# Optimization experiments

Hardware: AMD Instinct MI355X
Metric: run time of the kernel (lower is better)

## Reference

```python
import jax, jax.numpy as jnp
import numpy as np
import math

D_MODEL = 512
EXPAND = 1
D_INNER = EXPAND * D_MODEL          # 512
HALF = D_INNER // 2                 # 256 per-branch channels
D_STATE = D_MODEL // 4 * EXPAND     # 128 (overrides d_state arg in __init__)
DT_RANK = math.ceil(D_MODEL / 16)   # 32
D_CONV = 4


def _dwconv_same(x, w):
    # x: (B, C, L), w: (C, 1, k); torch padding='same' for k=4 -> pad (left=1, right=2)
    k = w.shape[-1]
    total = k - 1
    left = total // 2
    return jax.lax.conv_general_dilated(
        x, w, window_strides=(1,), padding=[(left, total - left)],
        feature_group_count=w.shape[0], dimension_numbers=("NCH", "OIH", "NCH"))


def _sparse_approx(m):
    thr = jnp.max(m) * 0.1
    return jnp.sign(m) * jax.nn.relu(jnp.abs(m) - thr)


def _selective_scan(u, delta, A, Bc, Cc, D):
    # u, delta: (B, d, L); A: (d, n); Bc, Cc: (B, n, L); D: (d,)
    dT = jnp.moveaxis(delta, 2, 0)   # (L, B, d)
    uT = jnp.moveaxis(u, 2, 0)       # (L, B, d)
    BT = jnp.moveaxis(Bc, 2, 0)      # (L, B, n)
    CT = jnp.moveaxis(Cc, 2, 0)      # (L, B, n)

    def step(h, inputs):
        d_t, u_t, b_t, c_t = inputs                      # (B,d),(B,d),(B,n),(B,n)
        dA = jnp.exp(d_t[..., None] * A)                 # (B, d, n)
        dBu = d_t[..., None] * b_t[:, None, :] * u_t[..., None]
        h = dA * h + dBu                                 # (B, d, n)
        y = jnp.einsum("bdn,bn->bd", h, c_t)
        return h, y

    h0 = jnp.zeros((u.shape[0], u.shape[1], A.shape[1]), dtype=u.dtype)
    _, ys = jax.lax.scan(step, h0, (dT, uT, BT, CT))     # ys: (L, B, d)
    y = jnp.moveaxis(ys, 0, 2)                           # (B, d, L)
    return y + u * D[:, None]


def _branch(inph, in_w, cx_w, cz_w, xproj_w, dt_w, dt_b, out_w, A, D):
    # inph: (B, L, d_model)
    xz = jnp.swapaxes(inph @ in_w.T, 1, 2)   # (B, d_inner, L)
    x, z = xz[:, :HALF], xz[:, HALF:]
    x = jax.nn.silu(_dwconv_same(x, cx_w))   # (B, half, L); conv bias is False (True//2==0)
    z = jax.nn.silu(_dwconv_same(z, cz_w))
    x_dbl = jnp.swapaxes(x, 1, 2) @ xproj_w.T        # (B, L, dt_rank + 2n)
    dt = x_dbl[..., :DT_RANK] @ dt_w.T               # (B, L, half)
    dt = jnp.swapaxes(dt, 1, 2)                      # (B, half, L)
    Bc = jnp.swapaxes(x_dbl[..., DT_RANK:DT_RANK + D_STATE], 1, 2)   # (B, n, L)
    Cc = jnp.swapaxes(x_dbl[..., DT_RANK + D_STATE:], 1, 2)          # (B, n, L)
    Bc = _sparse_approx(Bc)
    Cc = _sparse_approx(Cc)
    delta = jax.nn.softplus(dt + dt_b[None, :, None])
    y = _selective_scan(x, delta, A, Bc, Cc, D)
    out = jnp.concatenate([y, z], axis=1)            # (B, d_inner, L)
    return jnp.swapaxes(out, 1, 2) @ out_w.T         # (B, L, d_model)


def setup_inputs() -> dict:
    key = jax.random.key(0)
    ks = jax.random.split(key, 16)
    B, L = 2, 2048
    s = lambda fan: 1.0 / np.sqrt(fan)

    inp = jax.random.normal(ks[0], (B, 2 * D_MODEL, L), jnp.float32)

    in_proj_w = jax.random.uniform(ks[1], (D_INNER, D_MODEL), jnp.float32, -s(D_MODEL), s(D_MODEL))
    x_proj_w = jax.random.uniform(ks[2], (DT_RANK + 2 * D_STATE, HALF), jnp.float32, -s(HALF), s(HALF))
    dt_init_std = DT_RANK ** (-0.5)
    dt_proj_w = jax.random.uniform(ks[3], (HALF, DT_RANK), jnp.float32, -dt_init_std, dt_init_std)
    out_proj_w = jax.random.uniform(ks[4], (D_MODEL, D_INNER), jnp.float32, -s(D_INNER), s(D_INNER))

    in_proj_2_w = jax.random.uniform(ks[5], (D_INNER, D_MODEL), jnp.float32, -s(D_MODEL), s(D_MODEL))
    x_proj_2_w = jax.random.uniform(ks[6], (DT_RANK + 2 * D_STATE, HALF), jnp.float32, -s(HALF), s(HALF))
    dt_proj_2_w = jax.random.uniform(ks[7], (HALF, DT_RANK), jnp.float32, -dt_init_std, dt_init_std)
    out_proj_2_w = jax.random.uniform(ks[8], (D_MODEL, D_INNER), jnp.float32, -s(D_INNER), s(D_INNER))

    # dt bias init: inverse-softplus of dt ~ LogUniform(1e-3, 1e-1), floor 1e-4
    def inv_softplus_dt(k):
        u = jax.random.uniform(k, (HALF,), jnp.float32)
        dt = jnp.exp(u * (np.log(0.1) - np.log(0.001)) + np.log(0.001))
        dt = jnp.clip(dt, 1e-4, None)
        return dt + jnp.log(-jnp.expm1(-dt))
    dt_proj_b = inv_softplus_dt(ks[9])
    dt_proj_2_b = inv_softplus_dt(ks[10])

    cs = 1.0 / np.sqrt(D_CONV)  # depthwise conv fan_in = 1*k
    conv_x_w = jax.random.uniform(ks[11], (HALF, 1, D_CONV), jnp.float32, -cs, cs)
    conv_z_w = jax.random.uniform(ks[12], (HALF, 1, D_CONV), jnp.float32, -cs, cs)
    conv_x_2_w = jax.random.uniform(ks[13], (HALF, 1, D_CONV), jnp.float32, -cs, cs)
    conv_z_2_w = jax.random.uniform(ks[14], (HALF, 1, D_CONV), jnp.float32, -cs, cs)

    A_log = jnp.log(jnp.broadcast_to(jnp.arange(1, D_STATE + 1, dtype=jnp.float32), (HALF, D_STATE)))
    D = jnp.ones((HALF,), jnp.float32)
    epsilon = jnp.array([0.01], jnp.float32)

    return dict(inp=inp, in_proj_w=in_proj_w, conv_x_w=conv_x_w, conv_z_w=conv_z_w,
                x_proj_w=x_proj_w, dt_proj_w=dt_proj_w, dt_proj_b=dt_proj_b, out_proj_w=out_proj_w,
                in_proj_2_w=in_proj_2_w, conv_x_2_w=conv_x_2_w, conv_z_2_w=conv_z_2_w,
                x_proj_2_w=x_proj_2_w, dt_proj_2_w=dt_proj_2_w, dt_proj_2_b=dt_proj_2_b,
                out_proj_2_w=out_proj_2_w, A_log=A_log, D=D, epsilon=epsilon)


def reference(inp, in_proj_w, conv_x_w, conv_z_w, x_proj_w, dt_proj_w, dt_proj_b, out_proj_w,
              in_proj_2_w, conv_x_2_w, conv_z_2_w, x_proj_2_w, dt_proj_2_w, dt_proj_2_b,
              out_proj_2_w, A_log, D, epsilon):
    # inp: (B, 2*d_model, L) -> split along dim 1, permute to (B, L, d_model)
    inpx = jnp.swapaxes(inp[:, :D_MODEL, :], 1, 2)
    inpy = jnp.swapaxes(inp[:, D_MODEL:, :], 1, 2)

    A_base = (1.0 + epsilon[0]) * (-jnp.exp(A_log))
    A1 = _sparse_approx(A_base)        # branch 1
    A2 = _sparse_approx(A1)            # branch 2 sparsifies the already-sparsified A

    out1 = _branch(inpx, in_proj_w, conv_x_w, conv_z_w, x_proj_w, dt_proj_w, dt_proj_b, out_proj_w, A1, D)
    out2 = _branch(inpy, in_proj_2_w, conv_x_2_w, conv_z_2_w, x_proj_2_w, dt_proj_2_w, dt_proj_2_b, out_proj_2_w, A2, D)
    return out1, out2
```

## Files before the change

kernel.cpp:

```cpp
#include <hip/hip_runtime.h>
#include <math.h>

constexpr int B_    = 2;
constexpr int L_    = 2048;
constexpr int NROW  = B_ * L_;
constexpr int MROW  = 2 * NROW;
constexpr int HALF_ = 256;
constexpr int DS_   = 128;

constexpr float LOG2E = 1.4426950408889634f;

constexpr size_t OFF_MINP = 0;
constexpr size_t OFF_BCMX = 32;
constexpr size_t OFF_XZ   = 64;
constexpr size_t OFF_YT   = OFF_XZ + (size_t)MROW * 256;
constexpr size_t OFF_XDBL = OFF_XZ + (size_t)MROW * 512;
constexpr size_t OFF_XS   = OFF_XDBL + (size_t)MROW * 288;
constexpr size_t OFF_BS   = OFF_XS  + (size_t)MROW * 256;
constexpr size_t OFF_CS   = OFF_BS  + (size_t)2 * NROW * 128;
constexpr size_t OFF_DTT  = OFF_CS  + (size_t)2 * NROW * 128;
constexpr size_t OFF_DUT  = OFF_DTT + (size_t)2 * 256 * 4096;
constexpr size_t OFF_UDT  = OFF_DUT + (size_t)2 * 256 * 4096;
constexpr size_t FLOAT_END = OFF_UDT + (size_t)2 * 256 * 4096;

constexpr size_t HOFF_XINH = 0;
constexpr size_t HOFF_XINL = HOFF_XINH + (size_t)MROW * 512;
constexpr size_t HOFF_YZH  = HOFF_XINH;
constexpr size_t HOFF_YZL  = HOFF_XINL;
constexpr size_t HOFF_XSH  = HOFF_XINL + (size_t)MROW * 512;
constexpr size_t HOFF_XSL  = HOFF_XSH  + (size_t)MROW * 256;
constexpr size_t HOFF_INWH = HOFF_XSL  + (size_t)MROW * 256;
constexpr size_t HOFF_INWL = HOFF_INWH + 524288;
constexpr size_t HOFF_XWH  = HOFF_INWL + 524288;
constexpr size_t HOFF_XWL  = HOFF_XWH  + 147456;
constexpr size_t HOFF_OUTWH= HOFF_XWL  + 147456;
constexpr size_t HOFF_OUTWL= HOFF_OUTWH+ 524288;

constexpr size_t WST_IN = 262144;
constexpr size_t WST_X  = 73728;

constexpr int PRE_MINA = 32;
constexpr int PRE_WSPL = (1196032 + 255) / 256;
constexpr int PRE_TIN  = 64 * 16 * 4;
constexpr int PRE_BLOCKS = PRE_MINA + PRE_WSPL + PRE_TIN;

typedef __bf16 bf16x8 __attribute__((ext_vector_type(8)));
typedef float  f32x4  __attribute__((ext_vector_type(4)));

__device__ __forceinline__ unsigned short bf16rn(float x) {
    unsigned u = __float_as_uint(x);
    unsigned r = (u + 0x7FFFu + ((u >> 16) & 1u)) >> 16;
    return (unsigned short)r;
}
__device__ __forceinline__ void split2(float x, unsigned short& h, unsigned short& l) {
    h = bf16rn(x);
    float hf = __uint_as_float(((unsigned)h) << 16);
    l = bf16rn(x - hf);
}

__device__ __forceinline__ float shrinkf(float v, float thr) {
    float a = fabsf(v) - thr;
    a = fmaxf(a, 0.0f);
    float r = copysignf(a, v);
    return (v == 0.0f) ? 0.0f : r;
}
__device__ __forceinline__ float siluf(float v) { return v / (1.0f + __expf(-v)); }
__device__ __forceinline__ float softplusf(float v) {
    return fmaxf(v, 0.0f) + log1pf(__expf(-fabsf(v)));
}
__device__ __forceinline__ float rlanef(float v, int l) {
    return __int_as_float(__builtin_amdgcn_readlane(__float_as_int(v), l));
}
__device__ __forceinline__ unsigned fkey(float f) {
    unsigned u = __float_as_uint(f);
    return (u >> 31) ? ~u : (u | 0x80000000u);
}
__device__ __forceinline__ float funkey(unsigned k) {
    unsigned u = (k >> 31) ? (k & 0x7FFFFFFFu) : ~k;
    return __uint_as_float(u);
}

__global__ __launch_bounds__(256) void pre_all(const float* __restrict__ A_log,
                                               const float* __restrict__ inp,
                                               const float* __restrict__ in_w0,
                                               const float* __restrict__ in_w1,
                                               const float* __restrict__ outw0,
                                               const float* __restrict__ outw1,
                                               const float* __restrict__ xw0,
                                               const float* __restrict__ xw1,
                                               float* __restrict__ ws,
                                               unsigned* __restrict__ bcmax,
                                               unsigned short* __restrict__ hb) {
    int bid = blockIdx.x;
    int tid = threadIdx.x;
    if (bid < PRE_MINA) {
        __shared__ float sbuf[8];
        int i = bid * 1024 + tid * 4;
        float4 v = *(const float4*)(A_log + i);
        float mv = fminf(fminf(v.x, v.y), fminf(v.z, v.w));
        #pragma unroll
        for (int off = 32; off > 0; off >>= 1) mv = fminf(mv, __shfl_xor(mv, off));
        if ((tid & 63) == 0) sbuf[tid >> 6] = mv;
        __syncthreads();
        if (tid == 0) {
            float r = fminf(fminf(sbuf[0], sbuf[1]), fminf(sbuf[2], sbuf[3]));
            ws[OFF_MINP + bid] = r;
        }
        if (bid == 0 && tid < 4) bcmax[tid] = 0u;
    } else if (bid < PRE_MINA + PRE_WSPL) {
        int i = (bid - PRE_MINA) * 256 + tid;
        if (i >= 1196032) return;
        const float* src;
        size_t hbase, lbase;
        int off;
        if (i < 1048576) {
            int t = i >> 18;
            off = i & 262143;
            src = (t == 0) ? in_w0 : (t == 1) ? in_w1 : (t == 2) ? outw0 : outw1;
            if (t < 2) { hbase = HOFF_INWH + (size_t)t * WST_IN;  lbase = HOFF_INWL + (size_t)t * WST_IN; }
            else       { hbase = HOFF_OUTWH + (size_t)(t - 2) * WST_IN; lbase = HOFF_OUTWL + (size_t)(t - 2) * WST_IN; }
        } else {
            int j = i - 1048576;
            int t = (j < (int)WST_X) ? 0 : 1;
            off = j - t * (int)WST_X;
            src = t ? xw1 : xw0;
            hbase = HOFF_XWH + (size_t)t * WST_X;
            lbase = HOFF_XWL + (size_t)t * WST_X;
        }
        unsigned short h, l;
        split2(src[off], h, l);
        hb[hbase + off] = h;
        hb[lbase + off] = l;
    } else {
        __shared__ float tile[32][33];
        int idx = bid - PRE_MINA - PRE_WSPL;
        int bx = idx & 63;
        int by = (idx >> 6) & 15;
        int z  = idx >> 10;
        int br = z >> 1;
        int b  = z & 1;
        int t0 = bx * 32;
        int m0 = by * 32;
        int tx = tid & 31;
        int ty = tid >> 5;
        #pragma unroll
        for (int k = 0; k < 4; k++) {
            tile[ty + 8 * k][tx] =
                inp[((size_t)b * 1024 + br * 512 + m0 + ty + 8 * k) * L_ + t0 + tx];
        }
        __syncthreads();
        #pragma unroll
        for (int k = 0; k < 4; k++) {
            size_t dst = ((size_t)br * NROW + (size_t)b * L_ + t0 + ty + 8 * k) * 512 + m0 + tx;
            unsigned short h, l;
            split2(tile[tx][ty + 8 * k], h, l);
            hb[HOFF_XINH + dst] = h;
            hb[HOFF_XINL + dst] = l;
        }
    }
}

template <int NGUARD, int DOMAX>
__global__ __launch_bounds__(256) void gemm_mfma(const unsigned short* __restrict__ Ah,
                                                 const unsigned short* __restrict__ Al, int lda,
                                                 const unsigned short* __restrict__ WhB,
                                                 const unsigned short* __restrict__ WlB,
                                                 size_t wstride,
                                                 float* __restrict__ C, int ldc,
                                                 int N, int K,
                                                 unsigned* __restrict__ bcmax) {
    __shared__ __align__(16) unsigned short sAh[128 * 40];
    __shared__ __align__(16) unsigned short sAl[128 * 40];
    __shared__ __align__(16) unsigned short sBh[64 * 40];
    __shared__ __align__(16) unsigned short sBl[64 * 40];
    int tid  = threadIdx.x;
    int wid  = tid >> 6;
    int lane = tid & 63;
    int fr   = lane & 15;
    int kg   = lane >> 4;
    int mblk = blockIdx.y * 128;
    int nblk = blockIdx.x * 64;
    int br   = (mblk >= NROW) ? 1 : 0;
    const unsigned short* Wh = WhB + (size_t)br * wstride;
    const unsigned short* Wl = WlB + (size_t)br * wstride;
    int srow = tid >> 2;
    int skp  = (tid & 3) * 8;

    f32x4 acc[2][4] = {};

    for (int k0 = 0; k0 < K; k0 += 32) {
        uint4 vah0 = *(const uint4*)(Ah + (size_t)(mblk + srow) * lda + k0 + skp);
        uint4 vah1 = *(const uint4*)(Ah + (size_t)(mblk + 64 + srow) * lda + k0 + skp);
        uint4 val0 = *(const uint4*)(Al + (size_t)(mblk + srow) * lda + k0 + skp);
        uint4 val1 = *(const uint4*)(Al + (size_t)(mblk + 64 + srow) * lda + k0 + skp);
        uint4 vbh = {0, 0, 0, 0}, vbl = {0, 0, 0, 0};
        if (!NGUARD || (nblk + srow) < N) {
            vbh = *(const uint4*)(Wh + (size_t)(nblk + srow) * K + k0 + skp);
            vbl = *(const uint4*)(Wl + (size_t)(nblk + srow) * K + k0 + skp);
        }
        __syncthreads();
        *(uint4*)(sAh + srow * 40 + skp) = vah0;
        *(uint4*)(sAh + (64 + srow) * 40 + skp) = vah1;
        *(uint4*)(sAl + srow * 40 + skp) = val0;
        *(uint4*)(sAl + (64 + srow) * 40 + skp) = val1;
        *(uint4*)(sBh + srow * 40 + skp) = vbh;
        *(uint4*)(sBl + srow * 40 + skp) = vbl;
        __syncthreads();

        bf16x8 ah0 = *(const bf16x8*)(sAh + (wid * 32 + fr) * 40 + kg * 8);
        bf16x8 ah1 = *(const bf16x8*)(sAh + (wid * 32 + 16 + fr) * 40 + kg * 8);
        bf16x8 al0 = *(const bf16x8*)(sAl + (wid * 32 + fr) * 40 + kg * 8);
        bf16x8 al1 = *(const bf16x8*)(sAl + (wid * 32 + 16 + fr) * 40 + kg * 8);
        #pragma unroll
        for (int nt = 0; nt < 4; nt++) {
            bf16x8 bh = *(const bf16x8*)(sBh + (nt * 16 + fr) * 40 + kg * 8);
            bf16x8 bl = *(const bf16x8*)(sBl + (nt * 16 + fr) * 40 + kg * 8);
            acc[0][nt] = __builtin_amdgcn_mfma_f32_16x16x32_bf16(ah0, bh, acc[0][nt], 0, 0, 0);
            acc[0][nt] = __builtin_amdgcn_mfma_f32_16x16x32_bf16(ah0, bl, acc[0][nt], 0, 0, 0);
            acc[0][nt] = __builtin_amdgcn_mfma_f32_16x16x32_bf16(al0, bh, acc[0][nt], 0, 0, 0);
            acc[1][nt] = __builtin_amdgcn_mfma_f32_16x16x32_bf16(ah1, bh, acc[1][nt], 0, 0, 0);
            acc[1][nt] = __builtin_amdgcn_mfma_f32_16x16x32_bf16(ah1, bl, acc[1][nt], 0, 0, 0);
            acc[1][nt] = __builtin_amdgcn_mfma_f32_16x16x32_bf16(al1, bh, acc[1][nt], 0, 0, 0);
        }
    }
    #pragma unroll
    for (int mt = 0; mt < 2; mt++) {
        #pragma unroll
        for (int nt = 0; nt < 4; nt++) {
            int col = nblk + nt * 16 + fr;
            if (NGUARD && col >= N) continue;
            #pragma unroll
            for (int r = 0; r < 4; r++) {
                int row = mblk + wid * 32 + mt * 16 + kg * 4 + r;
                C[(size_t)row * ldc + col] = acc[mt][nt][r];
            }
        }
    }
    if (DOMAX) {
        float mb = -INFINITY, mc = -INFINITY;
        #pragma unroll
        for (int nt = 0; nt < 4; nt++) {
            int c16 = nblk + nt * 16;
            if (c16 >= 32 && c16 < 160) {
                #pragma unroll
                for (int mt = 0; mt < 2; mt++)
                    #pragma unroll
                    for (int r = 0; r < 4; r++) mb = fmaxf(mb, acc[mt][nt][r]);
            } else if (c16 >= 160 && c16 < 288) {
                #pragma unroll
                for (int mt = 0; mt < 2; mt++)
                    #pragma unroll
                    for (int r = 0; r < 4; r++) mc = fmaxf(mc, acc[mt][nt][r]);
            }
        }
        #pragma unroll
        for (int off = 32; off > 0; off >>= 1) {
            mb = fmaxf(mb, __shfl_xor(mb, off));
            mc = fmaxf(mc, __shfl_xor(mc, off));
        }
        if (lane == 0) {
            if (mb > -INFINITY) atomicMax(bcmax + 2 * br,     fkey(mb));
            if (mc > -INFINITY) atomicMax(bcmax + 2 * br + 1, fkey(mc));
        }
    }
}

__global__ __launch_bounds__(256) void conv_silu_kernel(const float* __restrict__ xz,
                                                        float* __restrict__ xs,
                                                        unsigned short* __restrict__ xsh,
                                                        unsigned short* __restrict__ xsl,
                                                        unsigned short* __restrict__ yzh,
                                                        unsigned short* __restrict__ yzl,
                                                        const float* __restrict__ wx0,
                                                        const float* __restrict__ wx1,
                                                        const float* __restrict__ wz0,
                                                        const float* __restrict__ wz1) {
    int idx = blockIdx.x * 256 + threadIdx.x;
    int c   = idx & 255;
    int row = idx >> 8;
    int br  = row >> 12;
    int t   = row & (L_ - 1);
    const float* wx = br ? wx1 : wx0;
    const float* wz = br ? wz1 : wz0;
    float ax = 0.0f, az = 0.0f;
    #pragma unroll
    for (int j = 0; j < 4; j++) {
        int tt = t + j - 1;
        if (tt >= 0 && tt < L_) {
            const float* p = xz + (size_t)(row + j - 1) * 512;
            ax = fmaf(p[c], wx[c * 4 + j], ax);
            az = fmaf(p[c + 256], wz[c * 4 + j], az);
        }
    }
    float sx = siluf(ax);
    float sz = siluf(az);
    xs[(size_t)row * 256 + c] = sx;
    unsigned short h, l;
    split2(sx, h, l);
    xsh[(size_t)row * 256 + c] = h;
    xsl[(size_t)row * 256 + c] = l;
    split2(sz, h, l);
    yzh[(size_t)row * 512 + 256 + c] = h;
    yzl[(size_t)row * 512 + 256 + c] = l;
}

__global__ __launch_bounds__(256) void dtprep_shrink(const float* __restrict__ A, int lda,
                                                     const float* __restrict__ W0,
                                                     const float* __restrict__ W1,
                                                     const float* __restrict__ b0,
                                                     const float* __restrict__ b1,
                                                     const float* __restrict__ xs,
                                                     const float* __restrict__ Dvec,
                                                     float* __restrict__ dtT,
                                                     float* __restrict__ duT,
                                                     float* __restrict__ udT,
                                                     const unsigned* __restrict__ bcmax,
                                                     float* __restrict__ Bs,
                                                     float* __restrict__ Cs) {
    __shared__ float As[16][68];
    __shared__ float Ws[16][68];
    int tid = threadIdx.x;
    int kk = tid & 15;
    int rr = tid >> 4;
    int mblk = blockIdx.y * 64;
    int nblk = blockIdx.x * 64;
    int br = (mblk >= NROW) ? 1 : 0;
    const float* W    = br ? W1 : W0;
    const float* bias = br ? b1 : b0;
    float acc[4][4] = {};
    for (int k0 = 0; k0 < 32; k0 += 16) {
        #pragma unroll
        for (int j = 0; j < 4; j++) {
            As[kk][rr + 16 * j] = A[(size_t)(mblk + rr + 16 * j) * lda + k0 + kk];
        }
        #pragma unroll
        for (int j = 0; j < 4; j++) {
            Ws[kk][rr + 16 * j] = W[(size_t)(nblk + rr + 16 * j) * 32 + k0 + kk];
        }
        __syncthreads();
        int ty = tid >> 4;
        int tx = tid & 15;
        #pragma unroll
        for (int kq = 0; kq < 16; kq++) {
            float a0 = As[kq][ty * 4 + 0];
            float a1 = As[kq][ty * 4 + 1];
            float a2 = As[kq][ty * 4 + 2];
            float a3 = As[kq][ty * 4 + 3];
            float v0 = Ws[kq][tx * 4 + 0];
            float v1 = Ws[kq][tx * 4 + 1];
            float v2 = Ws[kq][tx * 4 + 2];
            float v3 = Ws[kq][tx * 4 + 3];
            acc[0][0] = fmaf(a0, v0, acc[0][0]); acc[0][1] = fmaf(a0, v1, acc[0][1]);
            acc[0][2] = fmaf(a0, v2, acc[0][2]); acc[0][3] = fmaf(a0, v3, acc[0][3]);
            acc[1][0] = fmaf(a1, v0, acc[1][0]); acc[1][1] = fmaf(a1, v1, acc[1][1]);
            acc[1][2] = fmaf(a1, v2, acc[1][2]); acc[1][3] = fmaf(a1, v3, acc[1][3]);
            acc[2][0] = fmaf(a2, v0, acc[2][0]); acc[2][1] = fmaf(a2, v1, acc[2][1]);
            acc[2][2] = fmaf(a2, v2, acc[2][2]); acc[2][3] = fmaf(a2, v3, acc[2][3]);
            acc[3][0] = fmaf(a3, v0, acc[3][0]); acc[3][1] = fmaf(a3, v1, acc[3][1]);
            acc[3][2] = fmaf(a3, v2, acc[3][2]); acc[3][3] = fmaf(a3, v3, acc[3][3]);
        }
        __syncthreads();
    }
    {
        int ty = tid >> 4;
        int tx = tid & 15;
        #pragma unroll
        for (int i = 0; i < 4; i++) {
            int m = mblk + ty * 4 + i;
            int mloc = m & (NROW - 1);
            #pragma unroll
            for (int j = 0; j < 4; j++) {
                int n = nblk + tx * 4 + j;
                float delta = softplusf(acc[i][j] + bias[n]);
                float u = xs[(size_t)m * 256 + n];
                size_t dst = ((size_t)br * 256 + n) * 4096 + mloc;
                dtT[dst] = delta * LOG2E;
                duT[dst] = delta * u;
                udT[dst] = u * Dvec[n];
            }
        }
    }
    {
        int q = blockIdx.x;
        int isC = q >> 1;
        int cbase = (q & 1) * 64;
        int xoff = isC ? (160 + cbase) : (32 + cbase);
        float thr = 0.1f * funkey(bcmax[2 * br + isC]);
        float* dstArr = isC ? Cs : Bs;
        int r = tid >> 2;
        int c0 = (tid & 3) * 16;
        const float* src = A + (size_t)(mblk + r) * lda + xoff + c0;
        float* dp = dstArr + (size_t)(mblk + r) * 128 + cbase + c0;
        #pragma unroll
        for (int i = 0; i < 16; i += 4) {
            float4 v = *(const float4*)(src + i);
            float4 o;
            o.x = shrinkf(v.x, thr);
            o.y = shrinkf(v.y, thr);
            o.z = shrinkf(v.z, thr);
            o.w = shrinkf(v.w, thr);
            *(float4*)(dp + i) = o;
        }
    }
}

__global__ __launch_bounds__(128) void scan3_kernel(float* __restrict__ ws,
                                                    const float* __restrict__ A_log,
                                                    const float* __restrict__ eps) {
    int blk  = blockIdx.x;
    int xcd  = blk & 7;
    int slot = blk >> 3;
    int combo = xcd >> 1;
    int d  = (xcd & 1) * 128 + slot;
    int br = combo >> 1;
    int b  = combo & 1;
    int tid = threadIdx.x;
    int lt  = tid & 63;

    float pv = ws[OFF_MINP + (tid & 31)];
    #pragma unroll
    for (int off = 16; off > 0; off >>= 1) pv = fminf(pv, __shfl_xor(pv, off));
    float e  = 1.0f + eps[0];
    float m1 = -e * __expf(pv);
    float t1 = 0.1f * m1;
    float t2 = 0.1f * shrinkf(m1, t1);
    float base = -e * __expf(A_log[d * 128 + tid]);
    float a = shrinkf(base, t1);
    if (br) a = shrinkf(a, t2);

    size_t dchain = ((size_t)br * 256 + d) * 4096 + (size_t)b * L_;
    const float* dtT = ws + OFF_DTT + dchain;
    const float* duT = ws + OFF_DUT + dchain;
    const float* udT = ws + OFF_UDT + dchain;
    const float* Bp  = ws + OFF_BS + ((size_t)br * NROW + (size_t)b * L_) * 128 + tid;
    const float* Cp  = ws + OFF_CS + ((size_t)br * NROW + (size_t)b * L_) * 128 + tid;
    float*       yTp = ws + OFF_YT + dchain;

    __shared__ float red[64 * 132];
    __shared__ float comb[64];

    float h = 0.0f;

    float Bb[2][8], Cb[2][8];
    float dt_c = dtT[lt];
    float du_c = duT[lt];
    float ud_c = udT[lt];
    float dt_n = 0.f, du_n = 0.f, ud_n = 0.f;
    #pragma unroll
    for (int j = 0; j < 8; j++) { Bb[0][j] = Bp[(size_t)j * 128];       Cb[0][j] = Cp[(size_t)j * 128]; }
    #pragma unroll
    for (int j = 0; j < 8; j++) { Bb[1][j] = Bp[(size_t)(8 + j) * 128]; Cb[1][j] = Cp[(size_t)(8 + j) * 128]; }

    for (int c = 0; c < 32; c++) {
        if (c < 31) {
            dt_n = dtT[(c + 1) * 64 + lt];
            du_n = duT[(c + 1) * 64 + lt];
            ud_n = udT[(c + 1) * 64 + lt];
        }
        #pragma unroll
        for (int m = 0; m < 8; m++) {
            const int cur = m & 1;
            #pragma unroll
            for (int j = 0; j < 8; j++) {
                const int tl = m * 8 + j;
                float dt2 = rlanef(dt_c, tl);
                float du  = rlanef(du_c, tl);
                float ev = __builtin_amdgcn_exp2f(dt2 * a);
                h = fmaf(ev, h, du * Bb[cur][j]);
                red[tl * 132 + tid] = h * Cb[cur][j];
            }
            int nb = c * 8 + m + 2;
            if (nb < 256) {
                #pragma unroll
                for (int j = 0; j < 8; j++) {
                    Bb[cur][j] = Bp[((size_t)nb * 8 + j) * 128];
                    Cb[cur][j] = Cp[((size_t)nb * 8 + j) * 128];
                }
            }
        }
        __syncthreads();
        {
            const float* rp = &red[(tid & 63) * 132 + (tid >> 6) * 64];
            float s0 = 0.f, s1 = 0.f, s2 = 0.f, s3 = 0.f;
            #pragma unroll
            for (int i = 0; i < 64; i += 4) {
                float4 v = *(const float4*)(rp + i);
                s0 += v.x; s1 += v.y; s2 += v.z; s3 += v.w;
            }
            float part = (s0 + s1) + (s2 + s3);
            if (tid >= 64) comb[tid - 64] = part;
            __syncthreads();
            if (tid < 64) yTp[c * 64 + tid] = part + comb[tid] + ud_c;
        }
        __syncthreads();
        dt_c = dt_n;
        du_c = du_n;
        ud_c = ud_n;
    }
}

__global__ __launch_bounds__(256) void transpose_yz_kernel(const float* __restrict__ yT,
                                                           unsigned short* __restrict__ yzh,
                                                           unsigned short* __restrict__ yzl) {
    __shared__ float tile[32][33];
    int br = blockIdx.z;
    int m0 = blockIdx.x * 32;
    int n0 = blockIdx.y * 32;
    int tx = threadIdx.x;
    int ty = threadIdx.y;
    #pragma unroll
    for (int k = 0; k < 4; k++) {
        tile[ty + 8 * k][tx] = yT[((size_t)br * 256 + m0 + ty + 8 * k) * 4096 + n0 + tx];
    }
    __syncthreads();
    #pragma unroll
    for (int k = 0; k < 4; k++) {
        size_t dst = ((size_t)br * NROW + n0 + ty + 8 * k) * 512 + m0 + tx;
        unsigned short h, l;
        split2(tile[tx][ty + 8 * k], h, l);
        yzh[dst] = h; yzl[dst] = l;
    }
}

extern "C" void kernel_launch(void* const* d_in, const int* in_sizes, int n_in,
                              void* d_out, int out_size, void* d_ws, size_t ws_size,
                              hipStream_t stream) {
    const float* inp   = (const float*)d_in[0];
    const float* in_w[2]  = {(const float*)d_in[1],  (const float*)d_in[8]};
    const float* cxw[2]   = {(const float*)d_in[2],  (const float*)d_in[9]};
    const float* czw[2]   = {(const float*)d_in[3],  (const float*)d_in[10]};
    const float* xw[2]    = {(const float*)d_in[4],  (const float*)d_in[11]};
    const float* dtw[2]   = {(const float*)d_in[5],  (const float*)d_in[12]};
    const float* dtb[2]   = {(const float*)d_in[6],  (const float*)d_in[13]};
    const float* outw[2]  = {(const float*)d_in[7],  (const float*)d_in[14]};
    const float* A_log = (const float*)d_in[15];
    const float* Dvec  = (const float*)d_in[16];
    const float* eps   = (const float*)d_in[17];
    float* out = (float*)d_out;
    float* ws  = (float*)d_ws;
    unsigned short* hb = (unsigned short*)(ws + FLOAT_END);
    unsigned* bcmax = (unsigned*)(ws + OFF_BCMX);

    pre_all<<<PRE_BLOCKS, 256, 0, stream>>>(
        A_log, inp, in_w[0], in_w[1], outw[0], outw[1], xw[0], xw[1],
        ws, bcmax, hb);

    gemm_mfma<0, 0><<<dim3(512 / 64, MROW / 128), 256, 0, stream>>>(
        hb + HOFF_XINH, hb + HOFF_XINL, 512,
        hb + HOFF_INWH, hb + HOFF_INWL, WST_IN,
        ws + OFF_XZ, 512, 512, 512, nullptr);

    conv_silu_kernel<<<(MROW * HALF_) / 256, 256, 0, stream>>>(
        ws + OFF_XZ, ws + OFF_XS, hb + HOFF_XSH, hb + HOFF_XSL,
        hb + HOFF_YZH, hb + HOFF_YZL, cxw[0], cxw[1], czw[0], czw[1]);

    gemm_mfma<1, 1><<<dim3((288 + 63) / 64, MROW / 128), 256, 0, stream>>>(
        hb + HOFF_XSH, hb + HOFF_XSL, 256,
        hb + HOFF_XWH, hb + HOFF_XWL, WST_X,
        ws + OFF_XDBL, 288, 288, 256, bcmax);

    dtprep_shrink<<<dim3(4, MROW / 64), 256, 0, stream>>>(
        ws + OFF_XDBL, 288, dtw[0], dtw[1], dtb[0], dtb[1],
        ws + OFF_XS, Dvec,
        ws + OFF_DTT, ws + OFF_DUT, ws + OFF_UDT,
        bcmax, ws + OFF_BS, ws + OFF_CS);

    scan3_kernel<<<dim3(1024), 128, 0, stream>>>(ws, A_log, eps);

    transpose_yz_kernel<<<dim3(256 / 32, NROW / 32, 2), dim3(32, 8), 0, stream>>>(
        ws + OFF_YT, hb + HOFF_YZH, hb + HOFF_YZL);

    gemm_mfma<0, 0><<<dim3(512 / 64, MROW / 128), 256, 0, stream>>>(
        hb + HOFF_YZH, hb + HOFF_YZL, 512,
        hb + HOFF_OUTWH, hb + HOFF_OUTWL, WST_IN,
        out, 512, 512, 512, nullptr);
}
```

Measured before the change: 341.1 us.

## Prefetch GEMM tiles, vectorize conv-silu, stage dtprep transposed stores through LDS

The MFMA GEMM now loads the next K-slice from global memory into registers while the current slice is consumed from shared memory, so load latency overlaps with compute. The conv+SiLU kernel handles four channels per thread with float4/ushort4 loads and stores and a quarter of the threads. dtprep transposes its three outputs through a shared-memory buffer so writes to the channel-major arrays become coalesced float4 stores instead of strided scalar stores. The costs are higher register pressure in the GEMM and extra LDS use plus barriers in dtprep.

```diff
diff --git a/kernel.cpp b/kernel.cpp
--- a/kernel.cpp
+++ b/kernel.cpp
@@ -185,27 +185,48 @@
     const unsigned short* Wl = WlB + (size_t)br * wstride;
     int srow = tid >> 2;
     int skp  = (tid & 3) * 8;
+    bool brow_ok = (!NGUARD) || ((nblk + srow) < N);
+
+    const unsigned short* pA0 = Ah + (size_t)(mblk + srow) * lda + skp;
+    const unsigned short* pA1 = Ah + (size_t)(mblk + 64 + srow) * lda + skp;
+    const unsigned short* pL0 = Al + (size_t)(mblk + srow) * lda + skp;
+    const unsigned short* pL1 = Al + (size_t)(mblk + 64 + srow) * lda + skp;
+    const unsigned short* pBh = Wh + (size_t)(nblk + srow) * K + skp;
+    const unsigned short* pBl = Wl + (size_t)(nblk + srow) * K + skp;
 
     f32x4 acc[2][4] = {};
 
+    uint4 rah0 = *(const uint4*)(pA0);
+    uint4 rah1 = *(const uint4*)(pA1);
+    uint4 ral0 = *(const uint4*)(pL0);
+    uint4 ral1 = *(const uint4*)(pL1);
+    uint4 rbh = {0, 0, 0, 0}, rbl = {0, 0, 0, 0};
+    if (brow_ok) {
+        rbh = *(const uint4*)(pBh);
+        rbl = *(const uint4*)(pBl);
+    }
+
     for (int k0 = 0; k0 < K; k0 += 32) {
-        uint4 vah0 = *(const uint4*)(Ah + (size_t)(mblk + srow) * lda + k0 + skp);
-        uint4 vah1 = *(const uint4*)(Ah + (size_t)(mblk + 64 + srow) * lda + k0 + skp);
-        uint4 val0 = *(const uint4*)(Al + (size_t)(mblk + srow) * lda + k0 + skp);
-        uint4 val1 = *(const uint4*)(Al + (size_t)(mblk + 64 + srow) * lda + k0 + skp);
-        uint4 vbh = {0, 0, 0, 0}, vbl = {0, 0, 0, 0};
-        if (!NGUARD || (nblk + srow) < N) {
-            vbh = *(const uint4*)(Wh + (size_t)(nblk + srow) * K + k0 + skp);
-            vbl = *(const uint4*)(Wl + (size_t)(nblk + srow) * K + k0 + skp);
-        }
-        __syncthreads();
-        *(uint4*)(sAh + srow * 40 + skp) = vah0;
-        *(uint4*)(sAh + (64 + srow) * 40 + skp) = vah1;
-        *(uint4*)(sAl + srow * 40 + skp) = val0;
-        *(uint4*)(sAl + (64 + srow) * 40 + skp) = val1;
-        *(uint4*)(sBh + srow * 40 + skp) = vbh;
-        *(uint4*)(sBl + srow * 40 + skp) = vbl;
-        __syncthreads();
+        __syncthreads();
+        *(uint4*)(sAh + srow * 40 + skp) = rah0;
+        *(uint4*)(sAh + (64 + srow) * 40 + skp) = rah1;
+        *(uint4*)(sAl + srow * 40 + skp) = ral0;
+        *(uint4*)(sAl + (64 + srow) * 40 + skp) = ral1;
+        *(uint4*)(sBh + srow * 40 + skp) = rbh;
+        *(uint4*)(sBl + srow * 40 + skp) = rbl;
+        __syncthreads();
+
+        int kn = k0 + 32;
+        if (kn < K) {
+            rah0 = *(const uint4*)(pA0 + kn);
+            rah1 = *(const uint4*)(pA1 + kn);
+            ral0 = *(const uint4*)(pL0 + kn);
+            ral1 = *(const uint4*)(pL1 + kn);
+            if (brow_ok) {
+                rbh = *(const uint4*)(pBh + kn);
+                rbl = *(const uint4*)(pBl + kn);
+            }
+        }
 
         bf16x8 ah0 = *(const bf16x8*)(sAh + (wid * 32 + fr) * 40 + kg * 8);
         bf16x8 ah1 = *(const bf16x8*)(sAh + (wid * 32 + 16 + fr) * 40 + kg * 8);
@@ -275,33 +296,50 @@
                                                         const float* __restrict__ wx1,
                                                         const float* __restrict__ wz0,
                                                         const float* __restrict__ wz1) {
-    int idx = blockIdx.x * 256 + threadIdx.x;
-    int c   = idx & 255;
-    int row = idx >> 8;
+    int gid = blockIdx.x * 256 + threadIdx.x;
+    int c4  = (gid & 63) << 2;
+    int row = gid >> 6;
     int br  = row >> 12;
     int t   = row & (L_ - 1);
     const float* wx = br ? wx1 : wx0;
     const float* wz = br ? wz1 : wz0;
-    float ax = 0.0f, az = 0.0f;
+    float4 wxv[4], wzv[4];
+    #pragma unroll
+    for (int k = 0; k < 4; k++) {
+        wxv[k] = *(const float4*)(wx + (c4 + k) * 4);
+        wzv[k] = *(const float4*)(wz + (c4 + k) * 4);
+    }
+    float4 ax = {0, 0, 0, 0}, az = {0, 0, 0, 0};
     #pragma unroll
     for (int j = 0; j < 4; j++) {
         int tt = t + j - 1;
         if (tt >= 0 && tt < L_) {
             const float* p = xz + (size_t)(row + j - 1) * 512;
-            ax = fmaf(p[c], wx[c * 4 + j], ax);
-            az = fmaf(p[c + 256], wz[c * 4 + j], az);
-        }
-    }
-    float sx = siluf(ax);
-    float sz = siluf(az);
-    xs[(size_t)row * 256 + c] = sx;
-    unsigned short h, l;
-    split2(sx, h, l);
-    xsh[(size_t)row * 256 + c] = h;
-    xsl[(size_t)row * 256 + c] = l;
-    split2(sz, h, l);
-    yzh[(size_t)row * 512 + 256 + c] = h;
-    yzl[(size_t)row * 512 + 256 + c] = l;
+            float4 vx = *(const float4*)(p + c4);
+            float4 vz = *(const float4*)(p + 256 + c4);
+            ax.x = fmaf(vx.x, ((const float*)&wxv[0])[j], ax.x);
+            ax.y = fmaf(vx.y, ((const float*)&wxv[1])[j], ax.y);
+            ax.z = fmaf(vx.z, ((const float*)&wxv[2])[j], ax.z);
+            ax.w = fmaf(vx.w, ((const float*)&wxv[3])[j], ax.w);
+            az.x = fmaf(vz.x, ((const float*)&wzv[0])[j], az.x);
+            az.y = fmaf(vz.y, ((const float*)&wzv[1])[j], az.y);
+            az.z = fmaf(vz.z, ((const float*)&wzv[2])[j], az.z);
+            az.w = fmaf(vz.w, ((const float*)&wzv[3])[j], az.w);
+        }
+    }
+    float4 sx, sz;
+    sx.x = siluf(ax.x); sx.y = siluf(ax.y); sx.z = siluf(ax.z); sx.w = siluf(ax.w);
+    sz.x = siluf(az.x); sz.y = siluf(az.y); sz.z = siluf(az.z); sz.w = siluf(az.w);
+    *(float4*)(xs + (size_t)row * 256 + c4) = sx;
+    ushort4 hx, lx, hz, lz;
+    split2(sx.x, hx.x, lx.x); split2(sx.y, hx.y, lx.y);
+    split2(sx.z, hx.z, lx.z); split2(sx.w, hx.w, lx.w);
+    split2(sz.x, hz.x, lz.x); split2(sz.y, hz.y, lz.y);
+    split2(sz.z, hz.z, lz.z); split2(sz.w, hz.w, lz.w);
+    *(ushort4*)(xsh + (size_t)row * 256 + c4) = hx;
+    *(ushort4*)(xsl + (size_t)row * 256 + c4) = lx;
+    *(ushort4*)(yzh + (size_t)row * 512 + 256 + c4) = hz;
+    *(ushort4*)(yzl + (size_t)row * 512 + 256 + c4) = lz;
 }
 
 __global__ __launch_bounds__(256) void dtprep_shrink(const float* __restrict__ A, int lda,
@@ -319,6 +357,7 @@
                                                      float* __restrict__ Cs) {
     __shared__ float As[16][68];
     __shared__ float Ws[16][68];
+    __shared__ float tb[64 * 68];
     int tid = threadIdx.x;
     int kk = tid & 15;
     int rr = tid >> 4;
@@ -361,23 +400,47 @@
         }
         __syncthreads();
     }
-    {
-        int ty = tid >> 4;
-        int tx = tid & 15;
+    int ty = tid >> 4;
+    int tx = tid & 15;
+    float dlt[4][4], uu[4][4];
+    #pragma unroll
+    for (int i = 0; i < 4; i++) {
+        int m = mblk + ty * 4 + i;
+        #pragma unroll
+        for (int j = 0; j < 4; j++) {
+            int n = nblk + tx * 4 + j;
+            dlt[i][j] = softplusf(acc[i][j] + bias[n]);
+            uu[i][j]  = xs[(size_t)m * 256 + n];
+        }
+    }
+    float Dv[4];
+    #pragma unroll
+    for (int j = 0; j < 4; j++) Dv[j] = Dvec[nblk + tx * 4 + j];
+
+    int mlocbase = mblk & (NROW - 1);
+    int nrd  = tid >> 2;
+    int mc   = (tid & 3) * 4;
+    size_t obase = ((size_t)br * 256 + nblk + nrd) * 4096 + mlocbase;
+    #pragma unroll
+    for (int pass = 0; pass < 3; pass++) {
+        __syncthreads();
         #pragma unroll
         for (int i = 0; i < 4; i++) {
-            int m = mblk + ty * 4 + i;
-            int mloc = m & (NROW - 1);
             #pragma unroll
             for (int j = 0; j < 4; j++) {
-                int n = nblk + tx * 4 + j;
-                float delta = softplusf(acc[i][j] + bias[n]);
-                float u = xs[(size_t)m * 256 + n];
-                size_t dst = ((size_t)br * 256 + n) * 4096 + mloc;
-                dtT[dst] = delta * LOG2E;
-                duT[dst] = delta * u;
-                udT[dst] = u * Dvec[n];
+                float v = (pass == 0) ? dlt[i][j] * LOG2E
+                        : (pass == 1) ? dlt[i][j] * uu[i][j]
+                                      : uu[i][j] * Dv[j];
+                tb[(tx * 4 + j) * 68 + ty * 4 + i] = v;
             }
+        }
+        __syncthreads();
+        float* dst = (pass == 0) ? dtT : (pass == 1) ? duT : udT;
+        #pragma unroll
+        for (int it = 0; it < 4; it++) {
+            int cc = mc + it * 16;
+            float4 v = *(const float4*)(tb + nrd * 68 + cc);
+            *(float4*)(dst + obase + cc) = v;
         }
     }
     {
@@ -550,7 +613,7 @@
         hb + HOFF_INWH, hb + HOFF_INWL, WST_IN,
         ws + OFF_XZ, 512, 512, 512, nullptr);
 
-    conv_silu_kernel<<<(MROW * HALF_) / 256, 256, 0, stream>>>(
+    conv_silu_kernel<<<(MROW * 64) / 256, 256, 0, stream>>>(
         ws + OFF_XZ, ws + OFF_XS, hb + HOFF_XSH, hb + HOFF_XSL,
         hb + HOFF_YZH, hb + HOFF_YZL, cxw[0], cxw[1], czw[0], czw[1]);
 
```

After: 326.0 us. 1.05x faster.
